# Optimization experiments

Measured on AMD Instinct MI355X. Metric: run time of the kernel, lower is better.

The kernel has to match this reference:

```python
import jax, jax.numpy as jnp
import numpy as np


def _embedding_distances(dictionary, x_flat):
    # dictionary: [D, C], x_flat: [T, C] -> [T, D]
    dict_norms = jnp.sum(dictionary * dictionary, axis=-1)          # [D]
    x_norms = jnp.sum(x_flat * x_flat, axis=-1)                     # [T]
    dots = jnp.einsum('tc,dc->td', x_flat, dictionary)              # [T, D]
    return -2.0 * dots + dict_norms[None, :] + x_norms[:, None]


def _quantize(x, dictionary):
    # x: [N, C, H, W]
    N, C, H, W = x.shape
    cl = jnp.transpose(x, (0, 2, 3, 1))                             # [N, H, W, C]
    diffs = _embedding_distances(dictionary, cl.reshape(-1, C))     # [NHW, D]
    idxs = jnp.argmin(diffs, axis=-1).reshape(N, H, W)              # [N, H, W]
    embedded = jnp.transpose(dictionary[idxs], (0, 3, 1, 2))        # [N, C, H, W]
    embedded_pt = jax.lax.stop_gradient(embedded) + (x - jax.lax.stop_gradient(x))
    return embedded, embedded_pt, idxs


def setup_inputs() -> dict:
    key = jax.random.key(0)
    k1, k2, k3 = jax.random.split(key, 3)
    N, C, H, W, D = 32, 256, 32, 32, 1024
    return {
        'inputs': jax.random.normal(k1, (N, C, H, W), dtype=jnp.float32),
        'inputs_thermal': jax.random.normal(k2, (N, C, H, W), dtype=jnp.float32),
        'dictionary': jax.random.normal(k3, (D, C), dtype=jnp.float32),
    }


def reference(inputs, inputs_thermal, dictionary):
    embedded, embedded_pt, idxs = _quantize(inputs, dictionary)
    embedded_t, embedded_pt_t, idxs_t = _quantize(inputs_thermal, dictionary)
    return (embedded, embedded_pt, idxs, embedded_t, embedded_pt_t, idxs_t)
```

## Files before the change

### kernel.cpp

```cpp
#include <hip/hip_runtime.h>

#define NB    32
#define CCH   256
#define HW    1024
#define NPIX  (NB*HW)
#define DDICT 1024

#define EMB_ELEMS  ((size_t)NB*CCH*HW)
#define SEC_ELEMS  (2*EMB_ELEMS + NPIX)

#define TPX  128
#define TD   128
#define NDT  (DDICT/TD)
#define BK   32
#define NKC  (CCH/BK)
#define NPH  (NDT*NKC)

#define TAU  0.05f

typedef __attribute__((ext_vector_type(8))) short bf16x8;
typedef __attribute__((ext_vector_type(4))) float f32x4;

__device__ inline ushort split_rne(float f, float& rest) {
    uint u = __float_as_uint(f);
    uint r = u + 0x7FFFu + ((u >> 16) & 1u);
    rest = f - __uint_as_float(r & 0xFFFF0000u);
    return (ushort)(r >> 16);
}

__device__ inline ushort rne_bf16(float f) {
    uint u = __float_as_uint(f);
    return (ushort)((u + 0x7FFFu + ((u >> 16) & 1u)) >> 16);
}

__device__ inline void gll16(const void* g, void* l) {
    __builtin_amdgcn_global_load_lds(
        (const __attribute__((address_space(1))) uint*)g,
        (__attribute__((address_space(3))) uint*)l,
        16, 0, 0);
}

__global__ void dict_prep_kernel(const float* __restrict__ dict,
                                 ushort* __restrict__ dHs,
                                 ushort* __restrict__ dMs,
                                 float* __restrict__ dictT,
                                 float* __restrict__ norms) {
    int d = blockIdx.x;
    int lane = threadIdx.x;
    float4 f = ((const float4*)(dict + (size_t)d * CCH))[lane];
    float v[4] = {f.x, f.y, f.z, f.w};
    ushort h[4], m[4];
#pragma unroll
    for (int i = 0; i < 4; ++i) {
        float r1;
        h[i] = split_rne(v[i], r1);
        m[i] = rne_bf16(r1);
    }
    int c0 = lane * 4;
    int kc = c0 >> 5, oct = (c0 >> 3) & 3, e0 = c0 & 7;
    int dt = d >> 7, dd = d & 127;
    int slot = (oct + (dd >> 1)) & 3;
    size_t base = ((size_t)(dt * NKC + kc)) * 4096 + dd * 32 + slot * 8 + e0;
    *(ushort4*)(dHs + base) = make_ushort4(h[0], h[1], h[2], h[3]);
    *(ushort4*)(dMs + base) = make_ushort4(m[0], m[1], m[2], m[3]);
#pragma unroll
    for (int j = 0; j < 4; ++j)
        dictT[(size_t)(c0 + j) * DDICT + d] = v[j];

    if (lane == 0) {
        const float4* row = (const float4*)(dict + (size_t)d * CCH);
        float s = 0.f;
#pragma unroll 8
        for (int i = 0; i < CCH / 4; ++i) {
            float4 w = row[i];
            s += w.x * w.x + w.y * w.y + w.z * w.z + w.w * w.w;
        }
        norms[d] = s;
    }
}

__global__ __launch_bounds__(512, 4)
void vq_mega_kernel(const float* __restrict__ x0,
                    const float* __restrict__ x1,
                    const ushort* __restrict__ dHs,
                    const ushort* __restrict__ dMs,
                    const float* __restrict__ norms,
                    const float* __restrict__ dict,
                    const float* __restrict__ dictT,
                    float* __restrict__ out) {
    __shared__ ushort Bs[2][2][4096];
    __shared__ float nrm_s[DDICT];
    __shared__ int   idx_s[TPX];
    __shared__ int   fl_list[TPX];
    __shared__ int   fl_cnt;
    __shared__ float xr[CCH];
    __shared__ float rd_s[4];
    __shared__ int   ri_s[4];
    __shared__ int   bi_s;

    const int t    = threadIdx.x;
    const int lane = t & 63;
    const int wv   = t >> 6;
    const int lx   = lane & 15;
    const int q    = lane >> 4;
    const int m0w  = wv * 16;
    const int z    = blockIdx.y;

    const int g0  = blockIdx.x * TPX;
    const int n   = g0 / HW;
    const int hw0 = g0 % HW;

    const float* x = z ? x1 : x0;
    float* out_base = out + (size_t)z * SEC_ELEMS;
    float* out_emb    = out_base;
    float* out_emb_pt = out_base + EMB_ELEMS;
    float* out_idx    = out_base + 2 * EMB_ELEMS;

    if (t == 0) fl_cnt = 0;
    *(float2*)(nrm_s + t * 2) = *(const float2*)(norms + t * 2);

    const float* xbase = x + (size_t)n * CCH * HW + hw0 + m0w + lx;
    bf16x8 Ah[8], Am[8];
#pragma unroll
    for (int kc = 0; kc < NKC; ++kc) {
        float a_f[8];
#pragma unroll
        for (int j = 0; j < 8; ++j)
            a_f[j] = xbase[(size_t)(kc * BK + q * 8 + j) * HW];
#pragma unroll
        for (int j = 0; j < 8; ++j) {
            float r1;
            ushort h = split_rne(a_f[j], r1);
            Ah[kc][j] = (short)h;
            Am[kc][j] = (short)rne_bf16(r1);
        }
    }

    auto stage = [&](int p, int b) {
#pragma unroll
        for (int plane = 0; plane < 2; ++plane) {
            const ushort* sp = (plane ? dMs : dHs) + (size_t)p * 4096;
            gll16(sp + t * 8, &Bs[b][plane][wv * 512]);
        }
    };

    __syncthreads();
    stage(0, 0);

    float b1r[4], b2r[4]; int i1r[4];
#pragma unroll
    for (int r = 0; r < 4; ++r) {
        b1r[r] = 3.0e38f; b2r[r] = 3.0e38f; i1r[r] = 0;
    }

    for (int dt = 0; dt < NDT; ++dt) {
        f32x4 acc[8] = {};
#pragma unroll
        for (int kc = 0; kc < NKC; ++kc) {
            const int p = dt * 8 + kc;
            asm volatile("s_waitcnt vmcnt(0)" ::: "memory");
            __builtin_amdgcn_s_barrier();
            if (p + 1 < NPH) stage(p + 1, (p + 1) & 1);

            const ushort* bb = &Bs[p & 1][0][0];
            __builtin_amdgcn_s_setprio(1);
#pragma unroll
            for (int ni = 0; ni < 8; ++ni) {
                int nn   = ni * 16 + lx;
                int slot = (q + (nn >> 1)) & 3;
                int off  = nn * 32 + slot * 8;
                bf16x8 Bh = *(const bf16x8*)(bb + off);
                bf16x8 Bm = *(const bf16x8*)(bb + 4096 + off);
                f32x4 c = acc[ni];
                c = __builtin_amdgcn_mfma_f32_16x16x32_bf16(Ah[kc], Bh, c, 0, 0, 0);
                c = __builtin_amdgcn_mfma_f32_16x16x32_bf16(Ah[kc], Bm, c, 0, 0, 0);
                c = __builtin_amdgcn_mfma_f32_16x16x32_bf16(Am[kc], Bh, c, 0, 0, 0);
                acc[ni] = c;
            }
            __builtin_amdgcn_s_setprio(0);
        }

        const int d0 = dt * TD;
        float nrm[8];
#pragma unroll
        for (int ni = 0; ni < 8; ++ni) nrm[ni] = nrm_s[d0 + ni * 16 + lx];

#pragma unroll
        for (int r = 0; r < 4; ++r) {
            float c1 = 3.0e38f, c2 = 3.0e38f; int ci = 0;
#pragma unroll
            for (int ni = 0; ni < 8; ++ni) {
                float dist = fmaf(-2.f, acc[ni][r], nrm[ni]);
                if (dist < c1)      { c2 = c1; c1 = dist; ci = ni * 16 + lx; }
                else if (dist < c2) { c2 = dist; }
            }
#pragma unroll
            for (int off = 1; off < 16; off <<= 1) {
                float o1 = __shfl_xor(c1, off);
                int   oi = __shfl_xor(ci, off);
                float o2 = __shfl_xor(c2, off);
                if (o1 < c1 || (o1 == c1 && oi < ci)) {
                    c2 = fminf(c1, o2); c1 = o1; ci = oi;
                } else {
                    c2 = fminf(c2, o1);
                }
            }
            if (c1 < b1r[r]) {
                b2r[r] = fminf(b1r[r], c2);
                b1r[r] = c1;
                i1r[r] = d0 + ci;
            } else {
                b2r[r] = fminf(b2r[r], c1);
            }
        }
    }

#pragma unroll
    for (int r = 0; r < 4; ++r) {
        if (lx == 0) {
            int loc = m0w + q * 4 + r;
            idx_s[loc] = i1r[r];
            out_idx[g0 + loc] = (float)i1r[r];
            if (b2r[r] - b1r[r] < TAU) {
                int s = atomicAdd(&fl_cnt, 1);
                fl_list[s] = loc;
            }
        }
    }
    __syncthreads();

    {
        const int pg = t & 31;
        const int cg = t >> 5;
        const int hwp = hw0 + pg * 4;
        const float* r0 = dict + (size_t)idx_s[pg * 4 + 0] * CCH;
        const float* r1 = dict + (size_t)idx_s[pg * 4 + 1] * CCH;
        const float* r2 = dict + (size_t)idx_s[pg * 4 + 2] * CCH;
        const float* r3 = dict + (size_t)idx_s[pg * 4 + 3] * CCH;
        const size_t obase = (size_t)n * CCH * HW + hwp;
#pragma unroll
        for (int cq = 0; cq < 4; ++cq) {
            int c = cg * 16 + cq * 4;
            float4 q0 = *(const float4*)(r0 + c);
            float4 q1 = *(const float4*)(r1 + c);
            float4 q2 = *(const float4*)(r2 + c);
            float4 q3 = *(const float4*)(r3 + c);
            float4 v0 = make_float4(q0.x, q1.x, q2.x, q3.x);
            float4 v1 = make_float4(q0.y, q1.y, q2.y, q3.y);
            float4 v2 = make_float4(q0.z, q1.z, q2.z, q3.z);
            float4 v3 = make_float4(q0.w, q1.w, q2.w, q3.w);
            *(float4*)(out_emb    + obase + (size_t)(c + 0) * HW) = v0;
            *(float4*)(out_emb_pt + obase + (size_t)(c + 0) * HW) = v0;
            *(float4*)(out_emb    + obase + (size_t)(c + 1) * HW) = v1;
            *(float4*)(out_emb_pt + obase + (size_t)(c + 1) * HW) = v1;
            *(float4*)(out_emb    + obase + (size_t)(c + 2) * HW) = v2;
            *(float4*)(out_emb_pt + obase + (size_t)(c + 2) * HW) = v2;
            *(float4*)(out_emb    + obase + (size_t)(c + 3) * HW) = v3;
            *(float4*)(out_emb_pt + obase + (size_t)(c + 3) * HW) = v3;
        }
    }

    const int nf = fl_cnt;
    for (int fi = 0; fi < nf; ++fi) {
        __syncthreads();
        const int g  = g0 + fl_list[fi];
        const int hw = g % HW;
        if (t < 256) xr[t] = x[(size_t)n * CCH * HW + (size_t)t * HW + hw];
        __syncthreads();

        if (t < 256) {
            float bd = 3.0e38f; int bi = 0;
#pragma unroll
            for (int dd = 0; dd < 4; ++dd) {
                int d = dd * 256 + t;
                float dot = 0.f;
#pragma unroll 8
                for (int k = 0; k < CCH; ++k)
                    dot = fmaf(xr[k], dictT[(size_t)k * DDICT + d], dot);
                float dist = fmaf(-2.f, dot, nrm_s[d]);
                if (dist < bd) { bd = dist; bi = d; }
            }
#pragma unroll
            for (int off = 1; off < 64; off <<= 1) {
                float od = __shfl_xor(bd, off);
                int   oi = __shfl_xor(bi, off);
                if (od < bd || (od == bd && oi < bi)) { bd = od; bi = oi; }
            }
            if (lane == 0) { rd_s[wv] = bd; ri_s[wv] = bi; }
        }
        __syncthreads();
        if (t == 0) {
            float fb = rd_s[0]; int fid = ri_s[0];
#pragma unroll
            for (int q2 = 1; q2 < 4; ++q2)
                if (rd_s[q2] < fb || (rd_s[q2] == fb && ri_s[q2] < fid)) {
                    fb = rd_s[q2]; fid = ri_s[q2];
                }
            bi_s = fid;
            out_idx[g] = (float)fid;
        }
        __syncthreads();
        if (t < 256) {
            float v = dict[(size_t)bi_s * CCH + t];
            size_t o = (size_t)n * CCH * HW + (size_t)t * HW + hw;
            out_emb[o]    = v;
            out_emb_pt[o] = v;
        }
    }
}

extern "C" void kernel_launch(void* const* d_in, const int* in_sizes, int n_in,
                              void* d_out, int out_size, void* d_ws, size_t ws_size,
                              hipStream_t stream) {
    const float* x0   = (const float*)d_in[0];
    const float* x1   = (const float*)d_in[1];
    const float* dict = (const float*)d_in[2];
    float* out = (float*)d_out;

    float*  norms = (float*)d_ws;
    ushort* dHs   = (ushort*)(norms + DDICT);
    ushort* dMs   = dHs + (size_t)DDICT * CCH;
    float*  dictT = (float*)(dMs + (size_t)DDICT * CCH);

    dict_prep_kernel<<<dim3(DDICT), dim3(64), 0, stream>>>(dict, dHs, dMs,
                                                           dictT, norms);

    vq_mega_kernel<<<dim3(NPIX / TPX, 2), dim3(512), 0, stream>>>(
        x0, x1, dHs, dMs, norms, dict, dictT, out);
}
```

Baseline: 432.6 us.

## Load-balance near-tie fp32 refinement via global work queue with batched pixels

Near-tie pixels flagged by the bf16-split MMA pass are no longer refined only by the block that found them. Each block appends them to a global per-input list, and all blocks claim and process them dynamically in batches of four. Each batch does an exact fp32 distance search in which every dictionary load is reused across four pixels. The aim is to remove the tail imbalance from blocks with many flagged pixels and to cut dictT memory traffic. In exchange it adds global atomics, spin-waiting on a done counter that relies on forward progress of all blocks, and workspace initialisation in the prep kernel.

```diff
diff --git a/kernel.cpp b/kernel.cpp
--- a/kernel.cpp
+++ b/kernel.cpp
@@ -15,8 +15,11 @@
 #define BK   32
 #define NKC  (CCH/BK)
 #define NPH  (NDT*NKC)
+#define NBLKZ (NPIX/TPX)
 
 #define TAU  0.05f
+
+#define RB   4
 
 typedef __attribute__((ext_vector_type(8))) short bf16x8;
 typedef __attribute__((ext_vector_type(4))) float f32x4;
@@ -44,9 +47,15 @@
                                  ushort* __restrict__ dHs,
                                  ushort* __restrict__ dMs,
                                  float* __restrict__ dictT,
-                                 float* __restrict__ norms) {
+                                 float* __restrict__ norms,
+                                 int* __restrict__ lists,
+                                 int* __restrict__ ctrs) {
     int d = blockIdx.x;
     int lane = threadIdx.x;
+    int gidx = d * 64 + lane;
+    lists[gidx] = -1;
+    if (gidx < 6) ctrs[gidx] = 0;
+
     float4 f = ((const float4*)(dict + (size_t)d * CCH))[lane];
     float v[4] = {f.x, f.y, f.z, f.w};
     ushort h[4], m[4];
@@ -87,16 +96,18 @@
                     const float* __restrict__ norms,
                     const float* __restrict__ dict,
                     const float* __restrict__ dictT,
+                    int* __restrict__ lists,
+                    int* __restrict__ ctrs,
                     float* __restrict__ out) {
     __shared__ ushort Bs[2][2][4096];
     __shared__ float nrm_s[DDICT];
     __shared__ int   idx_s[TPX];
-    __shared__ int   fl_list[TPX];
-    __shared__ int   fl_cnt;
-    __shared__ float xr[CCH];
-    __shared__ float rd_s[4];
-    __shared__ int   ri_s[4];
-    __shared__ int   bi_s;
+    __shared__ float xr[CCH][RB];
+    __shared__ float rd_s[4][RB];
+    __shared__ int   ri_s[4][RB];
+    __shared__ int   cb[RB];
+    __shared__ int   bi_s[RB];
+    __shared__ int   cnp;
 
     const int t    = threadIdx.x;
     const int lane = t & 63;
@@ -115,8 +126,11 @@
     float* out_emb    = out_base;
     float* out_emb_pt = out_base + EMB_ELEMS;
     float* out_idx    = out_base + 2 * EMB_ELEMS;
-
-    if (t == 0) fl_cnt = 0;
+    int* list  = lists + (size_t)z * NPIX;
+    int* alloc = ctrs + z;
+    int* claim = ctrs + 2 + z;
+    int* done  = ctrs + 4 + z;
+
     *(float2*)(nrm_s + t * 2) = *(const float2*)(norms + t * 2);
 
     const float* xbase = x + (size_t)n * CCH * HW + hw0 + m0w + lx;
@@ -222,8 +236,9 @@
             idx_s[loc] = i1r[r];
             out_idx[g0 + loc] = (float)i1r[r];
             if (b2r[r] - b1r[r] < TAU) {
-                int s = atomicAdd(&fl_cnt, 1);
-                fl_list[s] = loc;
+                int slot = atomicAdd(alloc, 1);
+                __hip_atomic_store(&list[slot], g0 + loc,
+                                   __ATOMIC_RELEASE, __HIP_MEMORY_SCOPE_AGENT);
             }
         }
     }
@@ -260,52 +275,104 @@
         }
     }
 
-    const int nf = fl_cnt;
-    for (int fi = 0; fi < nf; ++fi) {
+    __threadfence();
+    if (t == 0)
+        __hip_atomic_fetch_add(done, 1, __ATOMIC_RELEASE, __HIP_MEMORY_SCOPE_AGENT);
+
+    for (;;) {
+        if (t == 0) {
+            int s0 = atomicAdd(claim, RB);
+            int np = 0;
+            for (int i = 0; i < RB; ++i) {
+                int s = s0 + i, v;
+                for (;;) {
+                    v = __hip_atomic_load(&list[s], __ATOMIC_ACQUIRE,
+                                          __HIP_MEMORY_SCOPE_AGENT);
+                    if (v >= 0) break;
+                    if (__hip_atomic_load(done, __ATOMIC_ACQUIRE,
+                                          __HIP_MEMORY_SCOPE_AGENT) == NBLKZ) {
+                        v = __hip_atomic_load(&list[s], __ATOMIC_ACQUIRE,
+                                              __HIP_MEMORY_SCOPE_AGENT);
+                        break;
+                    }
+                }
+                if (v < 0) break;
+                cb[np++] = v;
+            }
+            for (int i = np; i < RB && np > 0; ++i) cb[i] = cb[np - 1];
+            cnp = np;
+        }
         __syncthreads();
-        const int g  = g0 + fl_list[fi];
-        const int hw = g % HW;
-        if (t < 256) xr[t] = x[(size_t)n * CCH * HW + (size_t)t * HW + hw];
+        const int np = cnp;
+        if (np > 0) {
+            {
+                const int p2 = t >> 7;
+                const int c0 = (t & 127) * 2;
+                const int g  = cb[p2];
+                const int n2 = g / HW, h2 = g % HW;
+                const float* xb = x + (size_t)n2 * CCH * HW + h2;
+                xr[c0][p2]     = xb[(size_t)c0 * HW];
+                xr[c0 + 1][p2] = xb[(size_t)(c0 + 1) * HW];
+            }
+            __syncthreads();
+
+            if (t < 256) {
+                float ac[4][RB] = {};
+                for (int k = 0; k < CCH; ++k) {
+                    f32x4 xv = *(const f32x4*)&xr[k][0];
+#pragma unroll
+                    for (int dd = 0; dd < 4; ++dd) {
+                        float v = dictT[(size_t)k * DDICT + dd * 256 + t];
+#pragma unroll
+                        for (int p2 = 0; p2 < RB; ++p2)
+                            ac[dd][p2] = fmaf(xv[p2], v, ac[dd][p2]);
+                    }
+                }
+#pragma unroll
+                for (int p2 = 0; p2 < RB; ++p2) {
+                    float bd = 3.0e38f; int bi = 0;
+#pragma unroll
+                    for (int dd = 0; dd < 4; ++dd) {
+                        int d = dd * 256 + t;
+                        float dist = fmaf(-2.f, ac[dd][p2], nrm_s[d]);
+                        if (dist < bd) { bd = dist; bi = d; }
+                    }
+#pragma unroll
+                    for (int off = 1; off < 64; off <<= 1) {
+                        float od = __shfl_xor(bd, off);
+                        int   oi = __shfl_xor(bi, off);
+                        if (od < bd || (od == bd && oi < bi)) { bd = od; bi = oi; }
+                    }
+                    if (lane == 0) { rd_s[wv][p2] = bd; ri_s[wv][p2] = bi; }
+                }
+            }
+            __syncthreads();
+            if (t < RB) {
+                float fb = rd_s[0][t]; int fi = ri_s[0][t];
+#pragma unroll
+                for (int q2 = 1; q2 < 4; ++q2)
+                    if (rd_s[q2][t] < fb ||
+                        (rd_s[q2][t] == fb && ri_s[q2][t] < fi)) {
+                        fb = rd_s[q2][t]; fi = ri_s[q2][t];
+                    }
+                bi_s[t] = fi;
+                out_idx[cb[t]] = (float)fi;
+            }
+            __syncthreads();
+            if (t < 256) {
+#pragma unroll
+                for (int p2 = 0; p2 < RB; ++p2) {
+                    const int g  = cb[p2];
+                    const int n2 = g / HW, h2 = g % HW;
+                    float v = dict[(size_t)bi_s[p2] * CCH + t];
+                    size_t o = (size_t)n2 * CCH * HW + (size_t)t * HW + h2;
+                    out_emb[o]    = v;
+                    out_emb_pt[o] = v;
+                }
+            }
+        }
         __syncthreads();
-
-        if (t < 256) {
-            float bd = 3.0e38f; int bi = 0;
-#pragma unroll
-            for (int dd = 0; dd < 4; ++dd) {
-                int d = dd * 256 + t;
-                float dot = 0.f;
-#pragma unroll 8
-                for (int k = 0; k < CCH; ++k)
-                    dot = fmaf(xr[k], dictT[(size_t)k * DDICT + d], dot);
-                float dist = fmaf(-2.f, dot, nrm_s[d]);
-                if (dist < bd) { bd = dist; bi = d; }
-            }
-#pragma unroll
-            for (int off = 1; off < 64; off <<= 1) {
-                float od = __shfl_xor(bd, off);
-                int   oi = __shfl_xor(bi, off);
-                if (od < bd || (od == bd && oi < bi)) { bd = od; bi = oi; }
-            }
-            if (lane == 0) { rd_s[wv] = bd; ri_s[wv] = bi; }
-        }
-        __syncthreads();
-        if (t == 0) {
-            float fb = rd_s[0]; int fid = ri_s[0];
-#pragma unroll
-            for (int q2 = 1; q2 < 4; ++q2)
-                if (rd_s[q2] < fb || (rd_s[q2] == fb && ri_s[q2] < fid)) {
-                    fb = rd_s[q2]; fid = ri_s[q2];
-                }
-            bi_s = fid;
-            out_idx[g] = (float)fid;
-        }
-        __syncthreads();
-        if (t < 256) {
-            float v = dict[(size_t)bi_s * CCH + t];
-            size_t o = (size_t)n * CCH * HW + (size_t)t * HW + hw;
-            out_emb[o]    = v;
-            out_emb_pt[o] = v;
-        }
+        if (np < RB) break;
     }
 }
 
@@ -321,10 +388,13 @@
     ushort* dHs   = (ushort*)(norms + DDICT);
     ushort* dMs   = dHs + (size_t)DDICT * CCH;
     float*  dictT = (float*)(dMs + (size_t)DDICT * CCH);
+    int*    lists = (int*)(dictT + (size_t)DDICT * CCH);
+    int*    ctrs  = lists + 2 * NPIX;
 
     dict_prep_kernel<<<dim3(DDICT), dim3(64), 0, stream>>>(dict, dHs, dMs,
-                                                           dictT, norms);
+                                                           dictT, norms,
+                                                           lists, ctrs);
 
     vq_mega_kernel<<<dim3(NPIX / TPX, 2), dim3(512), 0, stream>>>(
-        x0, x1, dHs, dMs, norms, dict, dictT, out);
-}
+        x0, x1, dHs, dMs, norms, dict, dictT, lists, ctrs, out);
+}
```

New measurement: 524.3 us. 21.2% more time.

## Batch fallback exact-distance recomputation over eight pixels per pass

Applied to the files above, without the earlier changes.

The exact fp32 fallback for pixels whose bf16 distance margin was ambiguous used to run once per pixel, reading the whole transposed dictionary each time with only 256 threads active. It now handles up to eight flagged pixels per pass: each dictionary value loaded from global memory is reused across eight accumulators, and all 512 threads take part. The pixel vectors are staged in the now-idle Bs shared buffer. This amortises dictionary reads and syncs over the batch, in exchange for more registers and some wasted work when fewer than eight pixels remain.

```diff
diff --git a/kernel.cpp b/kernel.cpp
--- a/kernel.cpp
+++ b/kernel.cpp
@@ -17,6 +17,8 @@
 #define NPH  (NDT*NKC)
 
 #define TAU  0.05f
+
+#define RB   8
 
 typedef __attribute__((ext_vector_type(8))) short bf16x8;
 typedef __attribute__((ext_vector_type(4))) float f32x4;
@@ -93,10 +95,9 @@
     __shared__ int   idx_s[TPX];
     __shared__ int   fl_list[TPX];
     __shared__ int   fl_cnt;
-    __shared__ float xr[CCH];
-    __shared__ float rd_s[4];
-    __shared__ int   ri_s[4];
-    __shared__ int   bi_s;
+    __shared__ float rd_s[8][RB];
+    __shared__ int   ri_s[8][RB];
+    __shared__ int   bi_s[RB];
 
     const int t    = threadIdx.x;
     const int lane = t & 63;
@@ -261,50 +262,77 @@
     }
 
     const int nf = fl_cnt;
-    for (int fi = 0; fi < nf; ++fi) {
-        __syncthreads();
-        const int g  = g0 + fl_list[fi];
-        const int hw = g % HW;
-        if (t < 256) xr[t] = x[(size_t)n * CCH * HW + (size_t)t * HW + hw];
-        __syncthreads();
-
-        if (t < 256) {
-            float bd = 3.0e38f; int bi = 0;
-#pragma unroll
-            for (int dd = 0; dd < 4; ++dd) {
-                int d = dd * 256 + t;
-                float dot = 0.f;
-#pragma unroll 8
-                for (int k = 0; k < CCH; ++k)
-                    dot = fmaf(xr[k], dictT[(size_t)k * DDICT + d], dot);
-                float dist = fmaf(-2.f, dot, nrm_s[d]);
-                if (dist < bd) { bd = dist; bi = d; }
-            }
-#pragma unroll
-            for (int off = 1; off < 64; off <<= 1) {
-                float od = __shfl_xor(bd, off);
-                int   oi = __shfl_xor(bi, off);
-                if (od < bd || (od == bd && oi < bi)) { bd = od; bi = oi; }
-            }
-            if (lane == 0) { rd_s[wv] = bd; ri_s[wv] = bi; }
-        }
-        __syncthreads();
-        if (t == 0) {
-            float fb = rd_s[0]; int fid = ri_s[0];
-#pragma unroll
-            for (int q2 = 1; q2 < 4; ++q2)
-                if (rd_s[q2] < fb || (rd_s[q2] == fb && ri_s[q2] < fid)) {
-                    fb = rd_s[q2]; fid = ri_s[q2];
-                }
-            bi_s = fid;
-            out_idx[g] = (float)fid;
-        }
-        __syncthreads();
-        if (t < 256) {
-            float v = dict[(size_t)bi_s * CCH + t];
-            size_t o = (size_t)n * CCH * HW + (size_t)t * HW + hw;
-            out_emb[o]    = v;
-            out_emb_pt[o] = v;
+    if (nf > 0) {
+        float (*xr_)[CCH] = (float(*)[CCH])(&Bs[0][0][0]);
+        for (int f0 = 0; f0 < nf; f0 += RB) {
+            const int np = min(RB, nf - f0);
+            __syncthreads();
+            {
+                const int p  = t >> 6;
+                const int pi = f0 + ((p < np) ? p : (np - 1));
+                const int g  = g0 + fl_list[pi];
+                const int hw = g % HW;
+                const float* xb = x + (size_t)n * CCH * HW + hw;
+                const int c0 = (t & 63) * 4;
+#pragma unroll
+                for (int j = 0; j < 4; ++j)
+                    xr_[p][c0 + j] = xb[(size_t)(c0 + j) * HW];
+            }
+            __syncthreads();
+
+            float ac[2][RB] = {};
+            for (int k = 0; k < CCH; ++k) {
+                float xp[RB];
+#pragma unroll
+                for (int p = 0; p < RB; ++p) xp[p] = xr_[p][k];
+#pragma unroll
+                for (int dd = 0; dd < 2; ++dd) {
+                    float v = dictT[(size_t)k * DDICT + dd * 512 + t];
+#pragma unroll
+                    for (int p = 0; p < RB; ++p)
+                        ac[dd][p] = fmaf(xp[p], v, ac[dd][p]);
+                }
+            }
+#pragma unroll
+            for (int p = 0; p < RB; ++p) {
+                float bd = 3.0e38f; int bi = 0;
+#pragma unroll
+                for (int dd = 0; dd < 2; ++dd) {
+                    int d = dd * 512 + t;
+                    float dist = fmaf(-2.f, ac[dd][p], nrm_s[d]);
+                    if (dist < bd) { bd = dist; bi = d; }
+                }
+#pragma unroll
+                for (int off = 1; off < 64; off <<= 1) {
+                    float od = __shfl_xor(bd, off);
+                    int   oi = __shfl_xor(bi, off);
+                    if (od < bd || (od == bd && oi < bi)) { bd = od; bi = oi; }
+                }
+                if (lane == 0) { rd_s[wv][p] = bd; ri_s[wv][p] = bi; }
+            }
+            __syncthreads();
+            if (t < RB) {
+                float fb = rd_s[0][t]; int fi = ri_s[0][t];
+#pragma unroll
+                for (int w2 = 1; w2 < 8; ++w2)
+                    if (rd_s[w2][t] < fb ||
+                        (rd_s[w2][t] == fb && ri_s[w2][t] < fi)) {
+                        fb = rd_s[w2][t]; fi = ri_s[w2][t];
+                    }
+                bi_s[t] = fi;
+                if (t < np) out_idx[g0 + fl_list[f0 + t]] = (float)fi;
+            }
+            __syncthreads();
+            if (t < 256) {
+                for (int p = 0; p < np; ++p) {
+                    const int g  = g0 + fl_list[f0 + p];
+                    const int hw = g % HW;
+                    float v = dict[(size_t)bi_s[p] * CCH + t];
+                    size_t o = (size_t)n * CCH * HW + (size_t)t * HW + hw;
+                    out_emb[o]    = v;
+                    out_emb_pt[o] = v;
+                }
+            }
         }
     }
 }
```

After: 347.9 us. -19.6%, faster.
